# Performance work log

Measured on AMD Instinct MI355X. Metric: run time of the kernel, lower is better.

Reference implementation:

```python
import jax, jax.numpy as jnp
import numpy as np

B, V, D, E, F, H, HD = 16, 1024, 16, 64, 16, 128, 64
GRAPH_LAYERS, FLOW_ITERS, DUAL_ITERS = 2, 10, 10
STEP, MOM, BIG = 0.01, 0.9, 1e9


def _build_graph():
    # circulant graph: node v's d-th out-neighbor is v + offs[d] (mod V); offsets paired (o, -o)
    offs = np.array([1, -1, 2, -2, 3, -3, 4, -4, 5, -5, 6, -6, 7, -7, 8, -8], dtype=np.int32)
    v = np.arange(V, dtype=np.int32)[:, None]
    d = np.broadcast_to(np.arange(D, dtype=np.int32)[None, :], (V, D))
    adj = ((v + offs[None, :]) % V).astype(np.int32)
    inv_adj = ((v - offs[None, :]) % V).astype(np.int32)
    in_idx = np.stack([inv_adj, d], axis=-1)    # d-th incoming edge of v == out-edge (inv_adj[v,d], slot d)
    rev_idx = np.stack([adj, d], axis=-1)       # out-edge (v,d) is the d-th incoming edge of adj[v,d]
    opp_idx = np.stack([adj, d ^ 1], axis=-1)   # opposite edge (w->v) is slot d^1 at w (paired offsets)
    bt = lambda x: jnp.asarray(np.broadcast_to(x[None], (B,) + x.shape).copy())
    return bt(adj), bt(inv_adj), bt(in_idx), bt(rev_idx), bt(opp_idx)


def setup_inputs() -> dict:
    key = jax.random.key(0)
    ks = jax.random.split(key, 16)
    adj_lst, inv_adj_lst, in_indices, rev_indices, opp_indices = _build_graph()
    rn = lambda k, shape, scale=1.0: jax.random.normal(k, shape, dtype=jnp.float32) * scale
    s = lambda fan: 1.0 / float(np.sqrt(fan))
    return {
        'demands': rn(ks[0], (B, V, 1)),
        'node_features': rn(ks[1], (B, V, F)),
        'edge_lengths': jax.random.uniform(ks[2], (B, V, D), dtype=jnp.float32),
        'norm_edge_lengths': jax.random.uniform(ks[3], (B, V, D), dtype=jnp.float32),
        'node_emb': rn(ks[4], (V, E)),
        'W_enc': rn(ks[5], (E + F, H), s(E + F)), 'b_enc': jnp.zeros((H,), jnp.float32),
        'W_gat': rn(ks[6], (H, H), s(H)), 'b_gat': jnp.zeros((H,), jnp.float32),
        'a_gat': rn(ks[7], (H,), s(H)),
        'W_gru_x': rn(ks[8], (H, 3 * H), s(H)), 'W_gru_h': rn(ks[9], (H, 3 * H), s(H)),
        'b_gru': jnp.zeros((3 * H,), jnp.float32),
        'W_dec1': rn(ks[10], (2 * H, HD), s(2 * H)), 'b_dec1': jnp.zeros((HD,), jnp.float32),
        'W_dec2': rn(ks[11], (HD, 1), s(HD)), 'b_dec2': jnp.zeros((1,), jnp.float32),
        'W_dual1': rn(ks[12], (H, HD), s(H)), 'b_dual1': jnp.zeros((HD,), jnp.float32),
        'W_dual2': rn(ks[13], (HD, 1), s(HD)), 'b_dual2': jnp.zeros((1,), jnp.float32),
        'adj_lst': adj_lst, 'inv_adj_lst': inv_adj_lst,
        'in_indices': in_indices, 'rev_indices': rev_indices, 'opp_indices': opp_indices,
        'num_nodes': jnp.full((B,), V, dtype=jnp.int32),
    }


def _gather_nodes(values, idx, valid):
    # masked_gather with set_zero=True: values (B,V,H), idx (B,V,D) -> (B,V,D,H)
    bb = jnp.arange(values.shape[0])[:, None, None]
    g = values[bb, jnp.clip(idx, 0, values.shape[1] - 1)]
    return g * valid[..., None]


def _gather_edges(x, idx):
    # gather_nd into a (B,V,D,...) tensor; idx (B,V,D,2) = (node, slot), batch implicit
    bb = jnp.arange(x.shape[0])[:, None, None]
    return x[bb, idx[..., 0], idx[..., 1]]


def _sparsemax(z):
    n = z.shape[-1]
    zs = jnp.sort(z, axis=-1)[..., ::-1]
    k = jnp.arange(1, n + 1, dtype=z.dtype)
    zc = jnp.cumsum(zs, axis=-1)
    support = (1.0 + k * zs) > zc
    kz = jnp.sum(support, axis=-1, keepdims=True)
    tau = (jnp.take_along_axis(zc, kz - 1, axis=-1) - 1.0) / kz.astype(z.dtype)
    return jnp.maximum(z - tau, 0.0)


def _forward(demands, node_features, edge_lengths, norm_edge_lengths, node_emb, W_enc, b_enc,
             W_gat, b_gat, a_gat, W_gru_x, W_gru_h, b_gru, W_dec1, b_dec1, W_dec2, b_dec2,
             W_dual1, b_dual1, W_dual2, b_dual2,
             adj_lst, inv_adj_lst, in_indices, rev_indices, opp_indices, num_nodes):
    f32 = jnp.float32
    # embedding lookup with max_norm=1
    nrm = jnp.linalg.norm(node_emb, axis=-1, keepdims=True)
    emb = node_emb / jnp.maximum(nrm, 1.0)
    emb_b = jnp.broadcast_to(emb[None], (demands.shape[0], V, E))
    node_enc = jnp.concatenate([emb_b, node_features], axis=-1) @ W_enc + b_enc   # (B,V,H)
    mask = (adj_lst == num_nodes[:, None, None]).astype(f32)                       # 1 = padded slot
    valid = 1.0 - mask
    initial = _gather_nodes(node_enc, adj_lst, valid)                              # (B,V,D,H)
    h = initial
    for _ in range(GRAPH_LAYERS):
        # DirectionalGAT: per-edge transform, masked attention over slots, directional regather
        t = jnp.tanh(h @ W_gat + b_gat)                                            # (B,V,D,H)
        logits = jnp.einsum('bvdh,h->bvd', t, a_gat) - BIG * mask
        attn = jax.nn.softmax(logits, axis=-1)
        node_msg = jnp.einsum('bvd,bvdh->bvh', attn, t)                            # (B,V,H)
        msg = _gather_nodes(node_msg, adj_lst, valid)
        x = jnp.tanh(msg + initial)
        # GRU cell, shared weights over all edge states
        gx = x @ W_gru_x + b_gru
        gh = h @ W_gru_h
        z = jax.nn.sigmoid(gx[..., :H] + gh[..., :H])
        r = jax.nn.sigmoid(gx[..., H:2 * H] + gh[..., H:2 * H])
        cand = jnp.tanh(gx[..., 2 * H:] + r * gh[..., 2 * H:])
        h = z * h + (1.0 - z) * cand
    # decoder over (encoding, encoding + opposite-edge encoding)
    comb = h + _gather_edges(h, opp_indices)
    dec_in = jnp.concatenate([h, comb], axis=-1)
    nw = (jnp.tanh(dec_in @ W_dec1 + b_dec1) @ W_dec2 + b_dec2)[..., 0]            # (B,V,D)
    # destination attention: normalize over incoming edges, map back to outgoing layout
    inv_mask = (inv_adj_lst == num_nodes[:, None, None]).astype(f32)
    in_w = _gather_edges(nw, in_indices)
    dest_attn = jax.nn.softmax(in_w - BIG * inv_mask, axis=-1)
    nw = _gather_edges(dest_attn, rev_indices)
    pred = nw - BIG * mask
    normalized = _sparsemax(pred) * valid
    # iterative proportional min-cost-flow solver
    def mcf_step(flow, _):
        inflow = jnp.sum(_gather_edges(flow, in_indices), axis=-1, keepdims=True)  # (B,V,1)
        return normalized * jax.nn.relu(inflow - demands), None
    flow, _ = jax.lax.scan(mcf_step, jnp.zeros_like(normalized), None, length=FLOW_ITERS)
    flow_cost = jnp.sum(flow * flow, axis=(1, 2))                                  # square cost fn
    # dual variables + dual flow (projected momentum gradient descent)
    node_states = jnp.sum(h, axis=2)                                               # (B,V,H)
    dual_vars = jax.nn.relu(jnp.tanh(node_states @ W_dual1 + b_dual1) @ W_dual2 + b_dual2)  # (B,V,1)
    dual = mask * dual_vars
    dual_tr = _gather_nodes(dual_vars, adj_lst, valid)[..., 0]
    dual_diff = dual_tr - dual                                                     # (B,V,D)
    def dual_step(carry, _):
        f, vel = carry
        grad = 2.0 * f + dual_diff                                                 # d/df [f^2 + dual_diff*f]
        vel = MOM * vel - STEP * grad
        f = jax.nn.relu(f + vel)
        return (f, vel), None
    (dual_flows, _), _ = jax.lax.scan(dual_step, (jnp.zeros_like(dual_diff), jnp.zeros_like(dual_diff)), None, length=DUAL_ITERS)
    dual_flows = dual_flows * valid
    dual_demand = jnp.sum(dual_vars * demands, axis=(1, 2))
    dual_cost = jnp.sum(dual_flows * dual_flows + dual_diff * dual_flows, axis=(1, 2)) - dual_demand
    return flow_cost - dual_cost                                                   # (B,) primal-dual gap loss


def reference(demands, node_features, edge_lengths, norm_edge_lengths, node_emb, W_enc, b_enc,
              W_gat, b_gat, a_gat, W_gru_x, W_gru_h, b_gru, W_dec1, b_dec1, W_dec2, b_dec2,
              W_dual1, b_dual1, W_dual2, b_dual2,
              adj_lst, inv_adj_lst, in_indices, rev_indices, opp_indices, num_nodes):
    return _forward(demands, node_features, edge_lengths, norm_edge_lengths, node_emb, W_enc, b_enc,
                    W_gat, b_gat, a_gat, W_gru_x, W_gru_h, b_gru, W_dec1, b_dec1, W_dec2, b_dec2,
                    W_dual1, b_dual1, W_dual2, b_dual2,
                    adj_lst, inv_adj_lst, in_indices, rev_indices, opp_indices, num_nodes)
```

## Files before the change

kernel.cpp:

```cpp
#include <hip/hip_runtime.h>
#include <hip/hip_bf16.h>

#define B 16
#define V 1024
#define D 16
#define E 64
#define F 16
#define H 128
#define HD 64
#define BV (B*V)
#define BVD (B*V*D)

#define OFF_HNB      0
#define OFF_NORM     (OFF_HNB + BV*H/2)
#define OFF_DV       (OFF_NORM + BVD)
#define OFF_WT       (OFF_DV + BV)
#define OFF_WTG      (OFF_WT + 65536)
#define OFF_WPQ      (OFF_WTG + 8192)
#define OFF_WU1T     (OFF_WPQ + 8192)
#define OFF_WENCT    (OFF_WU1T + 4096)

typedef __attribute__((ext_vector_type(8))) short bf16x8;
typedef __attribute__((ext_vector_type(4))) float f32x4;

__device__ __forceinline__ short f2bf(float f){
  __hip_bfloat16 b = __float2bfloat16(f);
  return *reinterpret_cast<short*>(&b);
}
__device__ __forceinline__ float bf2f(short s){
  __hip_bfloat16 b; *reinterpret_cast<short*>(&b) = s;
  return __bfloat162float(b);
}
__device__ __forceinline__ float frcp(float x){ return __builtin_amdgcn_rcpf(x); }
__device__ __forceinline__ float fsig(float x){ return frcp(1.f + __expf(-x)); }
__device__ __forceinline__ float ftanh(float x){
  float e = __expf(-2.f*fabsf(x));
  float r = (1.f - e)*frcp(1.f + e);
  return copysignf(r, x);
}

__global__ __launch_bounds__(256) void k_pre(const float* __restrict__ Wx, const float* __restrict__ Wh,
    const float* __restrict__ Wg, const float* __restrict__ W1, const float* __restrict__ Wu1,
    const float* __restrict__ Wenc,
    short* __restrict__ Wt, short* __restrict__ Wgt, short* __restrict__ Wpq,
    short* __restrict__ Wu1t, short* __restrict__ Wenct){
  int bid = blockIdx.x, tid = threadIdx.x;
  if (bid < 512){
    int n = bid, k = tid;
    int g = n >> 7, j = n & 127;
    float v;
    if (g == 0)      v = (k < 128) ? Wx[k*384 + j]       : Wh[(k-128)*384 + j];
    else if (g == 1) v = (k < 128) ? Wx[k*384 + 128 + j] : Wh[(k-128)*384 + 128 + j];
    else if (g == 2) v = (k < 128) ? Wx[k*384 + 256 + j] : 0.f;
    else             v = (k < 128) ? 0.f                 : Wh[(k-128)*384 + 256 + j];
    Wt[n*256 + k] = f2bf(v);
    return;
  }
  if (bid < 576){
    int idx = (bid-512)*256 + tid;
    int n = idx >> 7, k = idx & 127;
    Wgt[n*128 + k] = f2bf(Wg[k*128 + n]);
    return;
  }
  if (bid < 608){
    int idx = (bid-576)*256 + tid;
    int n = idx >> 7, k = idx & 127;
    float wb = W1[(k+128)*HD + n];
    float wa = W1[k*HD + n];
    Wpq[n*128 + k]      = f2bf(wa + wb);
    Wpq[(64+n)*128 + k] = f2bf(wb);
    return;
  }
  if (bid < 640){
    int idx = (bid-608)*256 + tid;
    int n = idx >> 7, k = idx & 127;
    Wu1t[n*128 + k] = f2bf(Wu1[k*HD + n]);
    return;
  }
  {
    int nn = (bid-640)*2 + (tid >> 7);
    int kk = tid & 127;
    if (kk < 96) Wenct[nn*96 + kk] = f2bf(kk < 80 ? Wenc[kk*128 + nn] : 0.f);
  }
}

__global__ __launch_bounds__(512,2) void k_mega(const float* __restrict__ emb, const float* __restrict__ nf,
    const short* __restrict__ Wenct, const float* __restrict__ benc, const int* __restrict__ adj,
    const short* __restrict__ Wgt, const float* __restrict__ bg, const float* __restrict__ ag,
    const short* __restrict__ Wt, const float* __restrict__ bgru, short* __restrict__ hout){
  __shared__ short NE[96][136];
  __shared__ short T[96][136];
  __shared__ short H1[80][136];
  __shared__ short X[80][136];
  __shared__ float Lp[8][96];
  __shared__ float Ls[96];
  __shared__ float nrmv[96];
  short (*As)[104] = reinterpret_cast<short(*)[104]>(&H1[0][0]);

  int tid = threadIdx.x;
  int blk = blockIdx.x;
  int b = blk >> 4;
  int n0 = (blk & 15) << 6;
  int w = tid >> 6, lane = tid & 63;
  int l15 = lane & 15, quad = lane >> 4;

  if (tid < 96){
    int v = (n0 - 16 + tid) & 1023;
    const float4* e4 = reinterpret_cast<const float4*>(&emb[v*E]);
    float ss = 0.f;
    #pragma unroll
    for (int q=0;q<16;q++){ float4 x = e4[q]; ss += x.x*x.x + x.y*x.y + x.z*x.z + x.w*x.w; }
    nrmv[tid] = frcp(fmaxf(sqrtf(ss), 1.f));
  }
  __syncthreads();
  for (int e=tid; e<96*16; e+=512){
    int r = e >> 4, q = e & 15;
    int v = (n0 - 16 + r) & 1023;
    float4 x = reinterpret_cast<const float4*>(&emb[v*E])[q];
    float iv = nrmv[r];
    short4 s; s.x=f2bf(x.x*iv); s.y=f2bf(x.y*iv); s.z=f2bf(x.z*iv); s.w=f2bf(x.w*iv);
    *reinterpret_cast<short4*>(&As[r][q*4]) = s;
  }
  for (int e=tid; e<96*4; e+=512){
    int r = e >> 2, q = e & 3;
    int m = (b<<10) + ((n0 - 16 + r) & 1023);
    float4 x = reinterpret_cast<const float4*>(&nf[(long)m*F])[q];
    short4 s; s.x=f2bf(x.x); s.y=f2bf(x.y); s.z=f2bf(x.z); s.w=f2bf(x.w);
    *reinterpret_cast<short4*>(&As[r][64 + q*4]) = s;
    short4 z; z.x=0; z.y=0; z.z=0; z.w=0;
    *reinterpret_cast<short4*>(&As[r][80 + q*4]) = z;
  }
  __syncthreads();
  {
    f32x4 acc[6];
    #pragma unroll
    for (int mt=0;mt<6;mt++) acc[mt] = (f32x4){0.f,0.f,0.f,0.f};
    #pragma unroll
    for (int kc=0;kc<3;kc++){
      int k0 = kc*32;
      bf16x8 bfr = *reinterpret_cast<const bf16x8*>(&Wenct[(16*w + l15)*96 + k0 + quad*8]);
      #pragma unroll
      for (int mt=0;mt<6;mt++){
        bf16x8 a = *reinterpret_cast<const bf16x8*>(&As[16*mt + l15][k0 + quad*8]);
        acc[mt] = __builtin_amdgcn_mfma_f32_16x16x32_bf16(a, bfr, acc[mt], 0,0,0);
      }
    }
    int c = 16*w + l15;
    float bb = benc[c];
    #pragma unroll
    for (int mt=0;mt<6;mt++)
      #pragma unroll
      for (int reg=0;reg<4;reg++)
        NE[16*mt + quad*4 + reg][c] = f2bf(acc[mt][reg] + bb);
  }
  __syncthreads();
  {
    f32x4 acc[6];
    #pragma unroll
    for (int mt=0;mt<6;mt++) acc[mt] = (f32x4){0.f,0.f,0.f,0.f};
    #pragma unroll
    for (int kc=0;kc<4;kc++){
      int k0 = kc*32;
      bf16x8 bfr = *reinterpret_cast<const bf16x8*>(&Wgt[(16*w + l15)*128 + k0 + quad*8]);
      #pragma unroll
      for (int mt=0;mt<6;mt++){
        bf16x8 a = *reinterpret_cast<const bf16x8*>(&NE[16*mt + l15][k0 + quad*8]);
        acc[mt] = __builtin_amdgcn_mfma_f32_16x16x32_bf16(a, bfr, acc[mt], 0,0,0);
      }
    }
    int c = 16*w + l15;
    float bgc = bg[c], agc = ag[c];
    float lp[6][4];
    #pragma unroll
    for (int mt=0;mt<6;mt++)
      #pragma unroll
      for (int reg=0;reg<4;reg++){
        float t = ftanh(acc[mt][reg] + bgc);
        T[16*mt + quad*4 + reg][c] = f2bf(t);
        lp[mt][reg] = t * agc;
      }
    #pragma unroll
    for (int mt=0;mt<6;mt++)
      #pragma unroll
      for (int reg=0;reg<4;reg++){
        lp[mt][reg] += __shfl_xor(lp[mt][reg], 1);
        lp[mt][reg] += __shfl_xor(lp[mt][reg], 2);
        lp[mt][reg] += __shfl_xor(lp[mt][reg], 4);
        lp[mt][reg] += __shfl_xor(lp[mt][reg], 8);
      }
    if (l15 == 0){
      #pragma unroll
      for (int mt=0;mt<6;mt++)
        #pragma unroll
        for (int reg=0;reg<4;reg++)
          Lp[w][16*mt + quad*4 + reg] = lp[mt][reg];
    }
  }
  __syncthreads();
  if (tid < 96){
    float s = 0.f;
    #pragma unroll
    for (int i=0;i<8;i++) s += Lp[i][tid];
    Ls[tid] = s;
  }
  __syncthreads();
  if (tid < 320){
    int vl = tid >> 2, seg = tid & 3;
    int wg = (b<<10) + ((n0 - 8 + vl) & 1023);
    int li[16]; float at[16];
    float m = -1e30f;
    #pragma unroll
    for (int d=0; d<16; d++){
      int a = adj[wg*16 + d];
      li[d] = (a - n0 + 16) & 1023;
      m = fmaxf(m, Ls[li[d]]);
    }
    float s = 0.f;
    #pragma unroll
    for (int d=0; d<16; d++){ at[d] = __expf(Ls[li[d]] - m); s += at[d]; }
    float inv = frcp(s);
    #pragma unroll
    for (int d=0; d<16; d++) at[d] *= inv;
    #pragma unroll
    for (int c8=0; c8<4; c8++){
      int c = seg*32 + c8*8;
      float acc8[8] = {0,0,0,0,0,0,0,0};
      #pragma unroll 4
      for (int d=0; d<16; d++){
        bf16x8 tv = *reinterpret_cast<const bf16x8*>(&T[li[d]][c]);
        float a = at[d];
        #pragma unroll
        for (int q=0;q<8;q++) acc8[q] += a * bf2f(tv[q]);
      }
      bf16x8 nv = *reinterpret_cast<const bf16x8*>(&NE[vl + 8][c]);
      bf16x8 xv;
      #pragma unroll
      for (int q=0;q<8;q++) xv[q] = f2bf(ftanh(acc8[q] + bf2f(nv[q])));
      *reinterpret_cast<bf16x8*>(&X[vl][c]) = xv;
    }
  }
  __syncthreads();
  {
    f32x4 acc[5][4];
    #pragma unroll
    for (int mt=0;mt<5;mt++)
      #pragma unroll
      for (int g=0;g<4;g++) acc[mt][g] = (f32x4){0.f,0.f,0.f,0.f};
    for (int k8=0;k8<8;k8++){
      int k0 = k8*32;
      int gg = (k8 < 4) ? 2 : 3;
      int ncol = 16*w + l15;
      int koff = k0 + quad*8;
      bf16x8 bz = *reinterpret_cast<const bf16x8*>(&Wt[(ncol      )*256 + koff]);
      bf16x8 br = *reinterpret_cast<const bf16x8*>(&Wt[(ncol + 128)*256 + koff]);
      bf16x8 bc = *reinterpret_cast<const bf16x8*>(&Wt[(ncol + gg*128)*256 + koff]);
      #pragma unroll
      for (int mt=0;mt<5;mt++){
        bf16x8 a;
        if (k8 < 4) a = *reinterpret_cast<const bf16x8*>(&X[16*mt + l15][k0 + quad*8]);
        else        a = *reinterpret_cast<const bf16x8*>(&NE[16*mt + l15 + 8][k0 - 128 + quad*8]);
        acc[mt][0]  = __builtin_amdgcn_mfma_f32_16x16x32_bf16(a, bz, acc[mt][0], 0,0,0);
        acc[mt][1]  = __builtin_amdgcn_mfma_f32_16x16x32_bf16(a, br, acc[mt][1], 0,0,0);
        acc[mt][gg] = __builtin_amdgcn_mfma_f32_16x16x32_bf16(a, bc, acc[mt][gg], 0,0,0);
      }
    }
    int j = 16*w + l15;
    float bjz = bgru[j], bjr = bgru[128 + j], bjc = bgru[256 + j];
    #pragma unroll
    for (int mt=0;mt<5;mt++){
      #pragma unroll
      for (int reg=0;reg<4;reg++){
        int rl = 16*mt + quad*4 + reg;
        float z = fsig(acc[mt][0][reg] + bjz);
        float r = fsig(acc[mt][1][reg] + bjr);
        float cand = ftanh(acc[mt][2][reg] + bjc + r*acc[mt][3][reg]);
        float ho = bf2f(NE[rl + 8][j]);
        H1[rl][j] = f2bf(z*ho + (1.f - z)*cand);
      }
    }
  }
  __syncthreads();
  {
    f32x4 acc[5];
    #pragma unroll
    for (int mt=0;mt<5;mt++) acc[mt] = (f32x4){0.f,0.f,0.f,0.f};
    #pragma unroll
    for (int kc=0;kc<4;kc++){
      int k0 = kc*32;
      bf16x8 bfr = *reinterpret_cast<const bf16x8*>(&Wgt[(16*w + l15)*128 + k0 + quad*8]);
      #pragma unroll
      for (int mt=0;mt<5;mt++){
        bf16x8 a = *reinterpret_cast<const bf16x8*>(&H1[16*mt + l15][k0 + quad*8]);
        acc[mt] = __builtin_amdgcn_mfma_f32_16x16x32_bf16(a, bfr, acc[mt], 0,0,0);
      }
    }
    int c = 16*w + l15;
    float bgc = bg[c], agc = ag[c];
    float lp[5][4];
    #pragma unroll
    for (int mt=0;mt<5;mt++)
      #pragma unroll
      for (int reg=0;reg<4;reg++){
        float t = ftanh(acc[mt][reg] + bgc);
        T[16*mt + quad*4 + reg][c] = f2bf(t);
        lp[mt][reg] = t * agc;
      }
    #pragma unroll
    for (int mt=0;mt<5;mt++)
      #pragma unroll
      for (int reg=0;reg<4;reg++){
        lp[mt][reg] += __shfl_xor(lp[mt][reg], 1);
        lp[mt][reg] += __shfl_xor(lp[mt][reg], 2);
        lp[mt][reg] += __shfl_xor(lp[mt][reg], 4);
        lp[mt][reg] += __shfl_xor(lp[mt][reg], 8);
      }
    if (l15 == 0){
      #pragma unroll
      for (int mt=0;mt<5;mt++)
        #pragma unroll
        for (int reg=0;reg<4;reg++)
          Lp[w][16*mt + quad*4 + reg] = lp[mt][reg];
    }
  }
  __syncthreads();
  if (tid < 80){
    float s = 0.f;
    #pragma unroll
    for (int i=0;i<8;i++) s += Lp[i][tid];
    Ls[tid] = s;
  }
  __syncthreads();
  if (tid < 256){
    int vl = tid >> 2, seg = tid & 3;
    int vg = (b<<10) + n0 + vl;
    int li[16]; float at[16];
    float m = -1e30f;
    #pragma unroll
    for (int d=0; d<16; d++){
      int a = adj[vg*16 + d];
      li[d] = (a - n0 + 8) & 1023;
      m = fmaxf(m, Ls[li[d]]);
    }
    float s = 0.f;
    #pragma unroll
    for (int d=0; d<16; d++){ at[d] = __expf(Ls[li[d]] - m); s += at[d]; }
    float inv = frcp(s);
    #pragma unroll
    for (int d=0; d<16; d++) at[d] *= inv;
    #pragma unroll
    for (int c8=0; c8<4; c8++){
      int c = seg*32 + c8*8;
      float acc8[8] = {0,0,0,0,0,0,0,0};
      #pragma unroll 4
      for (int d=0; d<16; d++){
        bf16x8 tv = *reinterpret_cast<const bf16x8*>(&T[li[d]][c]);
        float a = at[d];
        #pragma unroll
        for (int q=0;q<8;q++) acc8[q] += a * bf2f(tv[q]);
      }
      bf16x8 nv = *reinterpret_cast<const bf16x8*>(&NE[vl + 16][c]);
      bf16x8 xv;
      #pragma unroll
      for (int q=0;q<8;q++) xv[q] = f2bf(ftanh(acc8[q] + bf2f(nv[q])));
      *reinterpret_cast<bf16x8*>(&X[vl][c]) = xv;
    }
  }
  __syncthreads();
  {
    f32x4 acc[4][4];
    #pragma unroll
    for (int mt=0;mt<4;mt++)
      #pragma unroll
      for (int g=0;g<4;g++) acc[mt][g] = (f32x4){0.f,0.f,0.f,0.f};
    for (int k8=0;k8<8;k8++){
      int k0 = k8*32;
      int gg = (k8 < 4) ? 2 : 3;
      int ncol = 16*w + l15;
      int koff = k0 + quad*8;
      bf16x8 bz = *reinterpret_cast<const bf16x8*>(&Wt[(ncol      )*256 + koff]);
      bf16x8 br = *reinterpret_cast<const bf16x8*>(&Wt[(ncol + 128)*256 + koff]);
      bf16x8 bc = *reinterpret_cast<const bf16x8*>(&Wt[(ncol + gg*128)*256 + koff]);
      #pragma unroll
      for (int mt=0;mt<4;mt++){
        bf16x8 a;
        if (k8 < 4) a = *reinterpret_cast<const bf16x8*>(&X[16*mt + l15][k0 + quad*8]);
        else        a = *reinterpret_cast<const bf16x8*>(&H1[16*mt + l15 + 8][k0 - 128 + quad*8]);
        acc[mt][0]  = __builtin_amdgcn_mfma_f32_16x16x32_bf16(a, bz, acc[mt][0], 0,0,0);
        acc[mt][1]  = __builtin_amdgcn_mfma_f32_16x16x32_bf16(a, br, acc[mt][1], 0,0,0);
        acc[mt][gg] = __builtin_amdgcn_mfma_f32_16x16x32_bf16(a, bc, acc[mt][gg], 0,0,0);
      }
    }
    __syncthreads();
    int j = 16*w + l15;
    float bjz = bgru[j], bjr = bgru[128 + j], bjc = bgru[256 + j];
    #pragma unroll
    for (int mt=0;mt<4;mt++){
      #pragma unroll
      for (int reg=0;reg<4;reg++){
        int rl = 16*mt + quad*4 + reg;
        float z = fsig(acc[mt][0][reg] + bjz);
        float r = fsig(acc[mt][1][reg] + bjr);
        float cand = ftanh(acc[mt][2][reg] + bjc + r*acc[mt][3][reg]);
        float ho = bf2f(H1[rl + 8][j]);
        X[rl][j] = f2bf(z*ho + (1.f - z)*cand);
      }
    }
  }
  __syncthreads();
  for (int idx=tid; idx<64*16; idx+=512){
    int r = idx >> 4, c8 = idx & 15;
    *reinterpret_cast<bf16x8*>(&hout[(long)((b<<10) + n0 + r)*128 + c8*8]) =
        *reinterpret_cast<const bf16x8*>(&X[r][c8*8]);
  }
}

__global__ __launch_bounds__(512,2) void k_decdas(const short* __restrict__ hn, const int* __restrict__ adj,
    const int* __restrict__ invadj, const short* __restrict__ Wpq, const float* __restrict__ b1,
    const float* __restrict__ W2, const float* __restrict__ b2_,
    const short* __restrict__ Wu1t, const float* __restrict__ bu1, const float* __restrict__ Wu2,
    const float* __restrict__ bu2_, float* __restrict__ norm_, float* __restrict__ dv){
  __shared__ short Hs[112][136];
  __shared__ short PQb[112][132];
  __shared__ short NSs[64][136];
  __shared__ int adjL[64][16];
  __shared__ float dvp[64][4];
  __shared__ float b1s[64], w2s[64], bu1s[64], wu2s[64];
  int tid = threadIdx.x;
  int blk = blockIdx.x;
  int b = blk >> 4;
  int n0 = (blk & 15) << 6;
  if (tid < 64){ b1s[tid] = b1[tid]; w2s[tid] = W2[tid]; bu1s[tid] = bu1[tid]; wu2s[tid] = Wu2[tid]; }
  for (int idx=tid; idx<112*16; idx+=512){
    int r = idx >> 4, c8 = idx & 15;
    int g = (b << 10) + ((n0 - 24 + r) & 1023);
    *reinterpret_cast<bf16x8*>(&Hs[r][c8*8]) =
        *reinterpret_cast<const bf16x8*>(&hn[(long)g*128 + c8*8]);
  }
  for (int idx=tid; idx<1024; idx+=512){
    int r = idx >> 4, d = idx & 15;
    int a = adj[((b<<10) + n0 + r)*16 + d];
    adjL[r][d] = (a - n0 + 24) & 1023;
  }
  __syncthreads();
  int w = tid >> 6, lane = tid & 63;
  int l15 = lane & 15, quad = lane >> 4;
  {
    f32x4 acc[7];
    #pragma unroll
    for (int mt=0;mt<7;mt++) acc[mt] = (f32x4){0.f,0.f,0.f,0.f};
    #pragma unroll
    for (int kc=0;kc<4;kc++){
      int k0 = kc*32;
      bf16x8 bfr = *reinterpret_cast<const bf16x8*>(&Wpq[(16*w + l15)*128 + k0 + quad*8]);
      #pragma unroll
      for (int mt=0;mt<7;mt++){
        bf16x8 a = *reinterpret_cast<const bf16x8*>(&Hs[16*mt + l15][k0 + quad*8]);
        acc[mt] = __builtin_amdgcn_mfma_f32_16x16x32_bf16(a, bfr, acc[mt], 0,0,0);
      }
    }
    int c = 16*w + l15;
    #pragma unroll
    for (int mt=0;mt<7;mt++)
      #pragma unroll
      for (int reg=0;reg<4;reg++)
        PQb[16*mt + quad*4 + reg][c] = f2bf(acc[mt][reg]);
  }
  for (int idx=tid; idx<64*16; idx+=512){
    int r = idx >> 4, c8 = idx & 15;
    float acc8[8] = {0,0,0,0,0,0,0,0};
    #pragma unroll 4
    for (int d=0; d<16; d++){
      bf16x8 hv = *reinterpret_cast<const bf16x8*>(&Hs[adjL[r][d]][c8*8]);
      #pragma unroll
      for (int q=0;q<8;q++) acc8[q] += bf2f(hv[q]);
    }
    bf16x8 sv;
    #pragma unroll
    for (int q=0;q<8;q++) sv[q] = f2bf(acc8[q]);
    *reinterpret_cast<bf16x8*>(&NSs[r][c8*8]) = sv;
  }
  __syncthreads();
  if (w < 4){
    f32x4 acc[4];
    #pragma unroll
    for (int mt=0;mt<4;mt++) acc[mt] = (f32x4){0.f,0.f,0.f,0.f};
    #pragma unroll
    for (int kc=0;kc<4;kc++){
      int k0 = kc*32;
      bf16x8 bfr = *reinterpret_cast<const bf16x8*>(&Wu1t[(16*w + l15)*128 + k0 + quad*8]);
      #pragma unroll
      for (int mt=0;mt<4;mt++){
        bf16x8 a = *reinterpret_cast<const bf16x8*>(&NSs[16*mt + l15][k0 + quad*8]);
        acc[mt] = __builtin_amdgcn_mfma_f32_16x16x32_bf16(a, bfr, acc[mt], 0,0,0);
      }
    }
    int n = 16*w + l15;
    float bn = bu1s[n], wn = wu2s[n];
    #pragma unroll
    for (int mt=0;mt<4;mt++){
      #pragma unroll
      for (int reg=0;reg<4;reg++){
        float p = ftanh(acc[mt][reg] + bn) * wn;
        p += __shfl_xor(p, 1);
        p += __shfl_xor(p, 2);
        p += __shfl_xor(p, 4);
        p += __shfl_xor(p, 8);
        if (l15 == 0) dvp[16*mt + quad*4 + reg][w] = p;
      }
    }
  }
  __syncthreads();
  float* nws = reinterpret_cast<float*>(&Hs[0][0]);
  float b2v = b2_[0];
  for (int e = tid; e < 96*16; e += 512){
    int rr = e >> 4, d = e & 15;
    int wnode = (n0 + rr - 16) & 1023;
    int wg = (b<<10) + wnode;
    int a = adj[wg*16 + d];
    int al = (a - n0 + 24) & 1023;
    int wl = rr + 8;
    float p = 0.f;
    #pragma unroll 8
    for (int c=0;c<64;c++)
      p += ftanh(bf2f(PQb[al][c]) + bf2f(PQb[wl][64 + c]) + b1s[c]) * w2s[c];
    nws[rr*17 + d] = p + b2v;
  }
  __syncthreads();
  if (tid < 64){
    float val = dvp[tid][0]+dvp[tid][1]+dvp[tid][2]+dvp[tid][3];
    dv[(b<<10) + n0 + tid] = fmaxf(val + bu2_[0], 0.f);
  }
  float* datt = reinterpret_cast<float*>(&PQb[0][0]);
  if (tid < 80){
    int wnode = (n0 + tid - 8) & 1023;
    int wg = (b<<10) + wnode;
    float vals[16];
    float m = -1e30f;
    #pragma unroll
    for (int d=0; d<16; d++){
      int iv = invadj[wg*16 + d];
      int il = (iv - n0 + 16) & 1023;
      vals[d] = nws[il*17 + d];
      m = fmaxf(m, vals[d]);
    }
    float s = 0.f;
    #pragma unroll
    for (int d=0; d<16; d++){ vals[d] = __expf(vals[d]-m); s += vals[d]; }
    float inv = frcp(s);
    #pragma unroll
    for (int d=0; d<16; d++) datt[tid*17 + d] = vals[d]*inv;
  }
  __syncthreads();
  if (tid < 64){
    int vg = (b<<10) + n0 + tid;
    float z[16], s[16];
    #pragma unroll
    for (int d=0; d<16; d++){
      int al = adjL[tid][d] - 16;
      z[d] = datt[al*17 + d];
      s[d] = z[d];
    }
    #pragma unroll
    for (int k2 = 2; k2 <= 16; k2 <<= 1){
      #pragma unroll
      for (int jj = k2 >> 1; jj > 0; jj >>= 1){
        #pragma unroll
        for (int i = 0; i < 16; i++){
          int l = i ^ jj;
          if (l > i){
            bool up = ((i & k2) == 0);
            float a = s[i], bb = s[l];
            bool sw = up ? (a > bb) : (a < bb);
            if (sw){ s[i]=bb; s[l]=a; }
          }
        }
      }
    }
    float cs = 0.f, zcs = 0.f; int kz = 1;
    #pragma unroll
    for (int j=0;j<16;j++){
      float zj = s[15-j];
      cs += zj;
      if (1.f + (float)(j+1)*zj > cs){ kz = j+1; zcs = cs; }
    }
    float tau = (zcs - 1.f)/(float)kz;
    #pragma unroll
    for (int d=0; d<16; d++) norm_[(long)vg*16 + d] = fmaxf(z[d]-tau, 0.f);
  }
}

__global__ __launch_bounds__(1024) void k_flowfin(const float* __restrict__ norm_,
    const float* __restrict__ dem, const int* __restrict__ invadj, const float* __restrict__ dv,
    float* __restrict__ out){
  __shared__ float nrmS[V*17];
  __shared__ float sbuf[2][V];
  __shared__ float r1[16], r2[16], r3[16];
  int b = blockIdx.x, v = threadIdx.x;
  int gv = (b<<10) + v;
  {
    const float4* src = reinterpret_cast<const float4*>(&norm_[(long)gv*16]);
    #pragma unroll
    for (int q4=0; q4<4; q4++){
      float4 x = src[q4];
      nrmS[v*17 + q4*4+0] = x.x; nrmS[v*17 + q4*4+1] = x.y;
      nrmS[v*17 + q4*4+2] = x.z; nrmS[v*17 + q4*4+3] = x.w;
    }
  }
  int iv[16];
  #pragma unroll
  for (int d4=0; d4<4; d4++){
    int4 i4 = reinterpret_cast<const int4*>(&invadj[(long)gv*16])[d4];
    iv[d4*4+0]=i4.x; iv[d4*4+1]=i4.y; iv[d4*4+2]=i4.z; iv[d4*4+3]=i4.w;
  }
  float dm = dem[gv];
  sbuf[0][v] = 0.f;
  __syncthreads();
  float nrg[16]; float nr2 = 0.f;
  #pragma unroll
  for (int d=0; d<16; d++){
    nrg[d] = nrmS[iv[d]*17 + d];
    float nv = nrmS[v*17 + d];
    nr2 += nv*nv;
  }
  int p = 0;
  float s = 0.f;
  for (int it=0; it<10; it++){
    float inflow = 0.f;
    #pragma unroll
    for (int d=0; d<16; d++) inflow += nrg[d]*sbuf[p][iv[d]];
    s = fmaxf(inflow - dm, 0.f);
    sbuf[1-p][v] = s;
    p ^= 1;
    __syncthreads();
  }
  float partF = nr2 * s * s;
  float dvv = dv[gv];
  float f = 0.f, vel = 0.f;
  #pragma unroll
  for (int it=0; it<10; it++){
    float g = 2.f*f + dvv;
    vel = 0.9f*vel - 0.01f*g;
    f = fmaxf(f + vel, 0.f);
  }
  float partD = f*f + dvv*f;
  float partDD = dvv * dm;
  #pragma unroll
  for (int off=32; off>0; off>>=1){
    partF  += __shfl_down(partF, off);
    partD  += __shfl_down(partD, off);
    partDD += __shfl_down(partDD, off);
  }
  if ((v & 63) == 0){ r1[v>>6] = partF; r2[v>>6] = partD; r3[v>>6] = partDD; }
  __syncthreads();
  if (v == 0){
    float sf = 0.f, sd = 0.f, sdd = 0.f;
    #pragma unroll
    for (int i=0;i<16;i++){ sf += r1[i]; sd += r2[i]; sdd += r3[i]; }
    out[b] = sf - (16.f*sd - sdd);
  }
}

extern "C" void kernel_launch(void* const* d_in, const int* in_sizes, int n_in,
                              void* d_out, int out_size, void* d_ws, size_t ws_size,
                              hipStream_t stream){
  (void)in_sizes; (void)n_in; (void)out_size; (void)ws_size;
  const float* demands = (const float*)d_in[0];
  const float* nf      = (const float*)d_in[1];
  const float* emb     = (const float*)d_in[4];
  const float* Wenc    = (const float*)d_in[5];
  const float* benc    = (const float*)d_in[6];
  const float* Wgat    = (const float*)d_in[7];
  const float* bgat    = (const float*)d_in[8];
  const float* agat    = (const float*)d_in[9];
  const float* Wgx     = (const float*)d_in[10];
  const float* Wgh     = (const float*)d_in[11];
  const float* bgru    = (const float*)d_in[12];
  const float* Wd1     = (const float*)d_in[13];
  const float* bd1     = (const float*)d_in[14];
  const float* Wd2     = (const float*)d_in[15];
  const float* bd2     = (const float*)d_in[16];
  const float* Wu1     = (const float*)d_in[17];
  const float* bu1     = (const float*)d_in[18];
  const float* Wu2     = (const float*)d_in[19];
  const float* bu2     = (const float*)d_in[20];
  const int* adj       = (const int*)d_in[21];
  const int* invadj    = (const int*)d_in[22];

  float* ws    = (float*)d_ws;
  short* hnB   = (short*)(ws + OFF_HNB);
  float* nrm   = ws + OFF_NORM;
  float* dv    = ws + OFF_DV;
  short* wt    = (short*)(ws + OFF_WT);
  short* wtg   = (short*)(ws + OFF_WTG);
  short* wpq   = (short*)(ws + OFF_WPQ);
  short* wu1t  = (short*)(ws + OFF_WU1T);
  short* wenct = (short*)(ws + OFF_WENCT);

  k_pre<<<704, 256, 0, stream>>>(Wgx, Wgh, Wgat, Wd1, Wu1, Wenc, wt, wtg, wpq, wu1t, wenct);
  k_mega<<<BV/64, 512, 0, stream>>>(emb, nf, wenct, benc, adj, wtg, bgat, agat, wt, bgru, hnB);
  k_decdas<<<BV/64, 512, 0, stream>>>(hnB, adj, invadj, wpq, bd1, Wd2, bd2,
                                      wu1t, bu1, Wu2, bu2, nrm, dv);
  k_flowfin<<<B, 1024, 0, stream>>>(nrm, demands, invadj, dv, (float*)d_out);
}
```

Measured before the change: 184.0 us.

## Shrink k_mega node tiles and split flow kernel into halo-tiled blocks

k_mega now handles 32 nodes per block instead of 64, which doubles the grid, shrinks shared memory and allows 4 blocks per CU. The per-batch flow iteration kernel, previously 16 blocks of 1024 threads, becomes 256 blocks of 256 threads. Each block recomputes an 80-node halo on each side so the 10 propagation steps stay exact within its tile, and the results are combined with an atomicAdd onto an output zeroed in k_pre. The cost is redundant halo computation in both kernels, plus a float atomic whose summation order is not deterministic.

```diff
diff --git a/kernel.cpp b/kernel.cpp
--- a/kernel.cpp
+++ b/kernel.cpp
@@ -43,8 +43,9 @@
     const float* __restrict__ Wg, const float* __restrict__ W1, const float* __restrict__ Wu1,
     const float* __restrict__ Wenc,
     short* __restrict__ Wt, short* __restrict__ Wgt, short* __restrict__ Wpq,
-    short* __restrict__ Wu1t, short* __restrict__ Wenct){
+    short* __restrict__ Wu1t, short* __restrict__ Wenct, float* __restrict__ outz){
   int bid = blockIdx.x, tid = threadIdx.x;
+  if (bid == 0 && tid < 16) outz[tid] = 0.f;
   if (bid < 512){
     int n = bid, k = tid;
     int g = n >> 7, j = n & 127;
@@ -84,27 +85,27 @@
   }
 }
 
-__global__ __launch_bounds__(512,2) void k_mega(const float* __restrict__ emb, const float* __restrict__ nf,
+__global__ __launch_bounds__(512,4) void k_mega(const float* __restrict__ emb, const float* __restrict__ nf,
     const short* __restrict__ Wenct, const float* __restrict__ benc, const int* __restrict__ adj,
     const short* __restrict__ Wgt, const float* __restrict__ bg, const float* __restrict__ ag,
     const short* __restrict__ Wt, const float* __restrict__ bgru, short* __restrict__ hout){
-  __shared__ short NE[96][136];
-  __shared__ short T[96][136];
-  __shared__ short H1[80][136];
-  __shared__ short X[80][136];
-  __shared__ float Lp[8][96];
-  __shared__ float Ls[96];
-  __shared__ float nrmv[96];
-  short (*As)[104] = reinterpret_cast<short(*)[104]>(&H1[0][0]);
+  __shared__ short NE[64][136];
+  __shared__ short T[64][136];
+  __shared__ short H1[48][136];
+  __shared__ short X[48][136];
+  __shared__ float Lp[8][64];
+  __shared__ float Ls[64];
+  __shared__ float nrmv[64];
+  short (*As)[136] = T;
 
   int tid = threadIdx.x;
   int blk = blockIdx.x;
-  int b = blk >> 4;
-  int n0 = (blk & 15) << 6;
+  int b = blk >> 5;
+  int n0 = (blk & 31) << 5;
   int w = tid >> 6, lane = tid & 63;
   int l15 = lane & 15, quad = lane >> 4;
 
-  if (tid < 96){
+  if (tid < 64){
     int v = (n0 - 16 + tid) & 1023;
     const float4* e4 = reinterpret_cast<const float4*>(&emb[v*E]);
     float ss = 0.f;
@@ -113,7 +114,7 @@
     nrmv[tid] = frcp(fmaxf(sqrtf(ss), 1.f));
   }
   __syncthreads();
-  for (int e=tid; e<96*16; e+=512){
+  for (int e=tid; e<64*16; e+=512){
     int r = e >> 4, q = e & 15;
     int v = (n0 - 16 + r) & 1023;
     float4 x = reinterpret_cast<const float4*>(&emb[v*E])[q];
@@ -121,7 +122,7 @@
     short4 s; s.x=f2bf(x.x*iv); s.y=f2bf(x.y*iv); s.z=f2bf(x.z*iv); s.w=f2bf(x.w*iv);
     *reinterpret_cast<short4*>(&As[r][q*4]) = s;
   }
-  for (int e=tid; e<96*4; e+=512){
+  for (int e=tid; e<64*4; e+=512){
     int r = e >> 2, q = e & 3;
     int m = (b<<10) + ((n0 - 16 + r) & 1023);
     float4 x = reinterpret_cast<const float4*>(&nf[(long)m*F])[q];
@@ -132,15 +133,15 @@
   }
   __syncthreads();
   {
-    f32x4 acc[6];
-    #pragma unroll
-    for (int mt=0;mt<6;mt++) acc[mt] = (f32x4){0.f,0.f,0.f,0.f};
+    f32x4 acc[4];
+    #pragma unroll
+    for (int mt=0;mt<4;mt++) acc[mt] = (f32x4){0.f,0.f,0.f,0.f};
     #pragma unroll
     for (int kc=0;kc<3;kc++){
       int k0 = kc*32;
       bf16x8 bfr = *reinterpret_cast<const bf16x8*>(&Wenct[(16*w + l15)*96 + k0 + quad*8]);
       #pragma unroll
-      for (int mt=0;mt<6;mt++){
+      for (int mt=0;mt<4;mt++){
         bf16x8 a = *reinterpret_cast<const bf16x8*>(&As[16*mt + l15][k0 + quad*8]);
         acc[mt] = __builtin_amdgcn_mfma_f32_16x16x32_bf16(a, bfr, acc[mt], 0,0,0);
       }
@@ -148,31 +149,31 @@
     int c = 16*w + l15;
     float bb = benc[c];
     #pragma unroll
-    for (int mt=0;mt<6;mt++)
+    for (int mt=0;mt<4;mt++)
       #pragma unroll
       for (int reg=0;reg<4;reg++)
         NE[16*mt + quad*4 + reg][c] = f2bf(acc[mt][reg] + bb);
   }
   __syncthreads();
   {
-    f32x4 acc[6];
-    #pragma unroll
-    for (int mt=0;mt<6;mt++) acc[mt] = (f32x4){0.f,0.f,0.f,0.f};
+    f32x4 acc[4];
+    #pragma unroll
+    for (int mt=0;mt<4;mt++) acc[mt] = (f32x4){0.f,0.f,0.f,0.f};
     #pragma unroll
     for (int kc=0;kc<4;kc++){
       int k0 = kc*32;
       bf16x8 bfr = *reinterpret_cast<const bf16x8*>(&Wgt[(16*w + l15)*128 + k0 + quad*8]);
       #pragma unroll
-      for (int mt=0;mt<6;mt++){
+      for (int mt=0;mt<4;mt++){
         bf16x8 a = *reinterpret_cast<const bf16x8*>(&NE[16*mt + l15][k0 + quad*8]);
         acc[mt] = __builtin_amdgcn_mfma_f32_16x16x32_bf16(a, bfr, acc[mt], 0,0,0);
       }
     }
     int c = 16*w + l15;
     float bgc = bg[c], agc = ag[c];
-    float lp[6][4];
-    #pragma unroll
-    for (int mt=0;mt<6;mt++)
+    float lp[4][4];
+    #pragma unroll
+    for (int mt=0;mt<4;mt++)
       #pragma unroll
       for (int reg=0;reg<4;reg++){
         float t = ftanh(acc[mt][reg] + bgc);
@@ -180,7 +181,7 @@
         lp[mt][reg] = t * agc;
       }
     #pragma unroll
-    for (int mt=0;mt<6;mt++)
+    for (int mt=0;mt<4;mt++)
       #pragma unroll
       for (int reg=0;reg<4;reg++){
         lp[mt][reg] += __shfl_xor(lp[mt][reg], 1);
@@ -190,21 +191,21 @@
       }
     if (l15 == 0){
       #pragma unroll
-      for (int mt=0;mt<6;mt++)
+      for (int mt=0;mt<4;mt++)
         #pragma unroll
         for (int reg=0;reg<4;reg++)
           Lp[w][16*mt + quad*4 + reg] = lp[mt][reg];
     }
   }
   __syncthreads();
-  if (tid < 96){
+  if (tid < 64){
     float s = 0.f;
     #pragma unroll
     for (int i=0;i<8;i++) s += Lp[i][tid];
     Ls[tid] = s;
   }
   __syncthreads();
-  if (tid < 320){
+  if (tid < 192){
     int vl = tid >> 2, seg = tid & 3;
     int wg = (b<<10) + ((n0 - 8 + vl) & 1023);
     int li[16]; float at[16];
@@ -241,9 +242,9 @@
   }
   __syncthreads();
   {
-    f32x4 acc[5][4];
-    #pragma unroll
-    for (int mt=0;mt<5;mt++)
+    f32x4 acc[3][4];
+    #pragma unroll
+    for (int mt=0;mt<3;mt++)
       #pragma unroll
       for (int g=0;g<4;g++) acc[mt][g] = (f32x4){0.f,0.f,0.f,0.f};
     for (int k8=0;k8<8;k8++){
@@ -255,7 +256,7 @@
       bf16x8 br = *reinterpret_cast<const bf16x8*>(&Wt[(ncol + 128)*256 + koff]);
       bf16x8 bc = *reinterpret_cast<const bf16x8*>(&Wt[(ncol + gg*128)*256 + koff]);
       #pragma unroll
-      for (int mt=0;mt<5;mt++){
+      for (int mt=0;mt<3;mt++){
         bf16x8 a;
         if (k8 < 4) a = *reinterpret_cast<const bf16x8*>(&X[16*mt + l15][k0 + quad*8]);
         else        a = *reinterpret_cast<const bf16x8*>(&NE[16*mt + l15 + 8][k0 - 128 + quad*8]);
@@ -267,7 +268,7 @@
     int j = 16*w + l15;
     float bjz = bgru[j], bjr = bgru[128 + j], bjc = bgru[256 + j];
     #pragma unroll
-    for (int mt=0;mt<5;mt++){
+    for (int mt=0;mt<3;mt++){
       #pragma unroll
       for (int reg=0;reg<4;reg++){
         int rl = 16*mt + quad*4 + reg;
@@ -281,24 +282,24 @@
   }
   __syncthreads();
   {
-    f32x4 acc[5];
-    #pragma unroll
-    for (int mt=0;mt<5;mt++) acc[mt] = (f32x4){0.f,0.f,0.f,0.f};
+    f32x4 acc[3];
+    #pragma unroll
+    for (int mt=0;mt<3;mt++) acc[mt] = (f32x4){0.f,0.f,0.f,0.f};
     #pragma unroll
     for (int kc=0;kc<4;kc++){
       int k0 = kc*32;
       bf16x8 bfr = *reinterpret_cast<const bf16x8*>(&Wgt[(16*w + l15)*128 + k0 + quad*8]);
       #pragma unroll
-      for (int mt=0;mt<5;mt++){
+      for (int mt=0;mt<3;mt++){
         bf16x8 a = *reinterpret_cast<const bf16x8*>(&H1[16*mt + l15][k0 + quad*8]);
         acc[mt] = __builtin_amdgcn_mfma_f32_16x16x32_bf16(a, bfr, acc[mt], 0,0,0);
       }
     }
     int c = 16*w + l15;
     float bgc = bg[c], agc = ag[c];
-    float lp[5][4];
-    #pragma unroll
-    for (int mt=0;mt<5;mt++)
+    float lp[3][4];
+    #pragma unroll
+    for (int mt=0;mt<3;mt++)
       #pragma unroll
       for (int reg=0;reg<4;reg++){
         float t = ftanh(acc[mt][reg] + bgc);
@@ -306,7 +307,7 @@
         lp[mt][reg] = t * agc;
       }
     #pragma unroll
-    for (int mt=0;mt<5;mt++)
+    for (int mt=0;mt<3;mt++)
       #pragma unroll
       for (int reg=0;reg<4;reg++){
         lp[mt][reg] += __shfl_xor(lp[mt][reg], 1);
@@ -316,21 +317,21 @@
       }
     if (l15 == 0){
       #pragma unroll
-      for (int mt=0;mt<5;mt++)
+      for (int mt=0;mt<3;mt++)
         #pragma unroll
         for (int reg=0;reg<4;reg++)
           Lp[w][16*mt + quad*4 + reg] = lp[mt][reg];
     }
   }
   __syncthreads();
-  if (tid < 80){
+  if (tid < 48){
     float s = 0.f;
     #pragma unroll
     for (int i=0;i<8;i++) s += Lp[i][tid];
     Ls[tid] = s;
   }
   __syncthreads();
-  if (tid < 256){
+  if (tid < 128){
     int vl = tid >> 2, seg = tid & 3;
     int vg = (b<<10) + n0 + vl;
     int li[16]; float at[16];
@@ -367,9 +368,9 @@
   }
   __syncthreads();
   {
-    f32x4 acc[4][4];
-    #pragma unroll
-    for (int mt=0;mt<4;mt++)
+    f32x4 acc[2][4];
+    #pragma unroll
+    for (int mt=0;mt<2;mt++)
       #pragma unroll
       for (int g=0;g<4;g++) acc[mt][g] = (f32x4){0.f,0.f,0.f,0.f};
     for (int k8=0;k8<8;k8++){
@@ -381,7 +382,7 @@
       bf16x8 br = *reinterpret_cast<const bf16x8*>(&Wt[(ncol + 128)*256 + koff]);
       bf16x8 bc = *reinterpret_cast<const bf16x8*>(&Wt[(ncol + gg*128)*256 + koff]);
       #pragma unroll
-      for (int mt=0;mt<4;mt++){
+      for (int mt=0;mt<2;mt++){
         bf16x8 a;
         if (k8 < 4) a = *reinterpret_cast<const bf16x8*>(&X[16*mt + l15][k0 + quad*8]);
         else        a = *reinterpret_cast<const bf16x8*>(&H1[16*mt + l15 + 8][k0 - 128 + quad*8]);
@@ -394,7 +395,7 @@
     int j = 16*w + l15;
     float bjz = bgru[j], bjr = bgru[128 + j], bjc = bgru[256 + j];
     #pragma unroll
-    for (int mt=0;mt<4;mt++){
+    for (int mt=0;mt<2;mt++){
       #pragma unroll
       for (int reg=0;reg<4;reg++){
         int rl = 16*mt + quad*4 + reg;
@@ -407,7 +408,7 @@
     }
   }
   __syncthreads();
-  for (int idx=tid; idx<64*16; idx+=512){
+  for (int idx=tid; idx<32*16; idx+=512){
     int r = idx >> 4, c8 = idx & 15;
     *reinterpret_cast<bf16x8*>(&hout[(long)((b<<10) + n0 + r)*128 + c8*8]) =
         *reinterpret_cast<const bf16x8*>(&X[r][c8*8]);
@@ -589,75 +590,84 @@
   }
 }
 
-__global__ __launch_bounds__(1024) void k_flowfin(const float* __restrict__ norm_,
+__global__ __launch_bounds__(256) void k_flowfin(const float* __restrict__ norm_,
     const float* __restrict__ dem, const int* __restrict__ invadj, const float* __restrict__ dv,
     float* __restrict__ out){
-  __shared__ float nrmS[V*17];
-  __shared__ float sbuf[2][V];
-  __shared__ float r1[16], r2[16], r3[16];
-  int b = blockIdx.x, v = threadIdx.x;
-  int gv = (b<<10) + v;
-  {
-    const float4* src = reinterpret_cast<const float4*>(&norm_[(long)gv*16]);
-    #pragma unroll
-    for (int q4=0; q4<4; q4++){
-      float4 x = src[q4];
-      nrmS[v*17 + q4*4+0] = x.x; nrmS[v*17 + q4*4+1] = x.y;
-      nrmS[v*17 + q4*4+2] = x.z; nrmS[v*17 + q4*4+3] = x.w;
-    }
-  }
-  int iv[16];
-  #pragma unroll
-  for (int d4=0; d4<4; d4++){
-    int4 i4 = reinterpret_cast<const int4*>(&invadj[(long)gv*16])[d4];
-    iv[d4*4+0]=i4.x; iv[d4*4+1]=i4.y; iv[d4*4+2]=i4.z; iv[d4*4+3]=i4.w;
-  }
-  float dm = dem[gv];
-  sbuf[0][v] = 0.f;
-  __syncthreads();
-  float nrg[16]; float nr2 = 0.f;
-  #pragma unroll
-  for (int d=0; d<16; d++){
-    nrg[d] = nrmS[iv[d]*17 + d];
-    float nv = nrmS[v*17 + d];
-    nr2 += nv*nv;
+  __shared__ float nrmS[224*17];
+  __shared__ float sbuf[2][224];
+  __shared__ float red[4];
+  int tid = threadIdx.x;
+  int blk = blockIdx.x;
+  int b = blk >> 4;
+  int t0 = (blk & 15) << 6;
+  for (int e=tid; e<224*4; e+=256){
+    int r = e >> 2, q4 = e & 3;
+    int v = (t0 - 80 + r) & 1023;
+    float4 x = reinterpret_cast<const float4*>(&norm_[(long)((b<<10) + v)*16])[q4];
+    nrmS[r*17 + q4*4+0] = x.x; nrmS[r*17 + q4*4+1] = x.y;
+    nrmS[r*17 + q4*4+2] = x.z; nrmS[r*17 + q4*4+3] = x.w;
+  }
+  bool act = tid < 224;
+  int r = tid;
+  float dm = 0.f; int gv = 0;
+  int ivl[16];
+  if (act){
+    int v = (t0 - 80 + r) & 1023;
+    gv = (b<<10) + v;
+    dm = dem[gv];
+    #pragma unroll
+    for (int d4=0; d4<4; d4++){
+      int4 i4 = reinterpret_cast<const int4*>(&invadj[(long)gv*16])[d4];
+      int t;
+      t = (i4.x - t0 + 80) & 1023; ivl[d4*4+0] = t < 224 ? t : 223;
+      t = (i4.y - t0 + 80) & 1023; ivl[d4*4+1] = t < 224 ? t : 223;
+      t = (i4.z - t0 + 80) & 1023; ivl[d4*4+2] = t < 224 ? t : 223;
+      t = (i4.w - t0 + 80) & 1023; ivl[d4*4+3] = t < 224 ? t : 223;
+    }
+    sbuf[0][r] = 0.f;
+  }
+  __syncthreads();
+  float nrg[16];
+  if (act){
+    #pragma unroll
+    for (int d=0; d<16; d++) nrg[d] = nrmS[ivl[d]*17 + d];
   }
   int p = 0;
   float s = 0.f;
   for (int it=0; it<10; it++){
-    float inflow = 0.f;
-    #pragma unroll
-    for (int d=0; d<16; d++) inflow += nrg[d]*sbuf[p][iv[d]];
-    s = fmaxf(inflow - dm, 0.f);
-    sbuf[1-p][v] = s;
+    if (act){
+      float inflow = 0.f;
+      #pragma unroll
+      for (int d=0; d<16; d++) inflow += nrg[d]*sbuf[p][ivl[d]];
+      s = fmaxf(inflow - dm, 0.f);
+      sbuf[1-p][r] = s;
+    }
     p ^= 1;
     __syncthreads();
   }
-  float partF = nr2 * s * s;
-  float dvv = dv[gv];
-  float f = 0.f, vel = 0.f;
+  float partF = 0.f, partD = 0.f, partDD = 0.f;
+  if (act && r >= 80 && r < 144){
+    float nr2 = 0.f;
+    #pragma unroll
+    for (int d=0; d<16; d++){ float nv = nrmS[r*17 + d]; nr2 += nv*nv; }
+    partF = nr2 * s * s;
+    float dvv = dv[gv];
+    float f = 0.f, vel = 0.f;
+    #pragma unroll
+    for (int it=0; it<10; it++){
+      float g = 2.f*f + dvv;
+      vel = 0.9f*vel - 0.01f*g;
+      f = fmaxf(f + vel, 0.f);
+    }
+    partD = f*f + dvv*f;
+    partDD = dvv * dm;
+  }
+  float val = partF - 16.f*partD + partDD;
   #pragma unroll
-  for (int it=0; it<10; it++){
-    float g = 2.f*f + dvv;
-    vel = 0.9f*vel - 0.01f*g;
-    f = fmaxf(f + vel, 0.f);
-  }
-  float partD = f*f + dvv*f;
-  float partDD = dvv * dm;
-  #pragma unroll
-  for (int off=32; off>0; off>>=1){
-    partF  += __shfl_down(partF, off);
-    partD  += __shfl_down(partD, off);
-    partDD += __shfl_down(partDD, off);
-  }
-  if ((v & 63) == 0){ r1[v>>6] = partF; r2[v>>6] = partD; r3[v>>6] = partDD; }
-  __syncthreads();
-  if (v == 0){
-    float sf = 0.f, sd = 0.f, sdd = 0.f;
-    #pragma unroll
-    for (int i=0;i<16;i++){ sf += r1[i]; sd += r2[i]; sdd += r3[i]; }
-    out[b] = sf - (16.f*sd - sdd);
-  }
+  for (int off=32; off>0; off>>=1) val += __shfl_down(val, off);
+  if ((tid & 63) == 0) red[tid>>6] = val;
+  __syncthreads();
+  if (tid == 0) atomicAdd(&out[b], red[0]+red[1]+red[2]+red[3]);
 }
 
 extern "C" void kernel_launch(void* const* d_in, const int* in_sizes, int n_in,
@@ -696,9 +706,10 @@
   short* wu1t  = (short*)(ws + OFF_WU1T);
   short* wenct = (short*)(ws + OFF_WENCT);
 
-  k_pre<<<704, 256, 0, stream>>>(Wgx, Wgh, Wgat, Wd1, Wu1, Wenc, wt, wtg, wpq, wu1t, wenct);
-  k_mega<<<BV/64, 512, 0, stream>>>(emb, nf, wenct, benc, adj, wtg, bgat, agat, wt, bgru, hnB);
+  k_pre<<<704, 256, 0, stream>>>(Wgx, Wgh, Wgat, Wd1, Wu1, Wenc, wt, wtg, wpq, wu1t, wenct,
+                                 (float*)d_out);
+  k_mega<<<BV/32, 512, 0, stream>>>(emb, nf, wenct, benc, adj, wtg, bgat, agat, wt, bgru, hnB);
   k_decdas<<<BV/64, 512, 0, stream>>>(hnB, adj, invadj, wpq, bd1, Wd2, bd2,
                                       wu1t, bu1, Wu2, bu2, nrm, dv);
-  k_flowfin<<<B, 1024, 0, stream>>>(nrm, demands, invadj, dv, (float*)d_out);
+  k_flowfin<<<B*16, 256, 0, stream>>>(nrm, demands, invadj, dv, (float*)d_out);
 }
```

Result: slower. 194.4 us (+5.7%).
